# Kernel optimization log

Measured on AMD Instinct MI355X. Metric: run time of the kernel, lower is better.

## Reference

```python
import jax, jax.numpy as jnp
import numpy as np

N, L, D, H = 2, 2048, 1024, 16
Dh = D // H          # 64
HIST = 2048          # history_len
SCALE = D ** 0.5     # note: module scales by sqrt(model_dim), not sqrt(head_dim)


def setup_inputs() -> dict:
    key = jax.random.key(0)
    ks = jax.random.split(key, 10)
    f = lambda k, s, sc=1.0: jax.random.normal(k, s, dtype=jnp.float32) * sc
    i = jnp.arange(L)
    causal = i[None, :] > i[:, None]            # mask future
    old = i[None, :] <= i[:, None] - HIST       # mask beyond history window
    mask = causal | old                          # True = masked, (L, L)
    return {
        "values": f(ks[0], (N, L, D)),
        "keys": f(ks[1], (N, L, D)),
        "query": f(ks[2], (N, L, D)),
        "origin_values": f(ks[3], (N, L, D)),
        "origin_keys": f(ks[4], (N, L, D)),
        "Wv": f(ks[5], (Dh, Dh), 0.1),
        "Wk": f(ks[6], (Dh, Dh), 0.1),
        "Wq": f(ks[7], (Dh, Dh), 0.1),
        "fc_w": f(ks[8], (D, D), 0.03),
        "fc_b": jnp.zeros((D,), dtype=jnp.float32),
        "mask": mask,
    }


def reference(values, keys, query, origin_values, origin_keys, Wv, Wk, Wq, fc_w, fc_b, mask):
    # forward(..., ref_sample=True): mfpca_attention path.
    # origin_keys/values are projected exactly as the prior ref_sample=False call stored them.
    split = lambda x: x.reshape(N, L, H, Dh)
    v = split(values) @ Wv.T        # (N, L, H, Dh)  torch Linear: x @ W^T, no bias
    k = split(keys) @ Wk.T
    q = split(query) @ Wq.T
    ov = split(origin_values) @ Wv.T
    ok = split(origin_keys) @ Wk.T

    energy = jnp.einsum('nqhd,nkhd->nhqk', q, ok)       # (N, H, L, L)
    samp_energy = jnp.einsum('nlhd,nlhd->nhl', q, k)    # (N, H, L)
    eye = jnp.eye(L, dtype=bool)
    # energy.diagonal().copy_(samp_energy)
    energy = jnp.where(eye, samp_energy[:, :, None, :], energy)
    energy = jnp.where(mask, jnp.float32(-1e20), energy)
    scores = jax.nn.softmax(energy / SCALE, axis=-1)
    diag_scores = jnp.diagonal(scores, axis1=2, axis2=3)    # (N, H, L)
    scores_nodiag = jnp.where(eye, 0.0, scores)
    # NOTE: original einsum output is indexed by l (not q) -- reproduced faithfully.
    origin_attention = jnp.einsum('nhql,nlhd->nlhd', scores_nodiag, ov)
    samp_attention = jnp.einsum('nhl,nlhd->nlhd', diag_scores, v)
    attention = (samp_attention + origin_attention).reshape(N, L, D)
    return attention @ fc_w.T + fc_b
```

## Files before the change

kernel.cpp:

```cpp
#include <hip/hip_runtime.h>

#define NB 2
#define LL 2048
#define DD 1024
#define HH 16
#define NHH (NB*HH)
#define LT (LL/64)
#define KT16 (LL/16)
#define CEXP 0.0450842200277801f

typedef __bf16 bf16x8 __attribute__((ext_vector_type(8)));
typedef unsigned short u16x8 __attribute__((ext_vector_type(8)));
typedef float f32x4 __attribute__((ext_vector_type(4)));

#define MFMA16 __builtin_amdgcn_mfma_f32_16x16x32_bf16
#define EXP2 __builtin_amdgcn_exp2f

__device__ __forceinline__ unsigned short f2bf(float f) {
    unsigned u = __float_as_uint(f);
    return (unsigned short)((u + 0x7fffu + ((u >> 16) & 1u)) >> 16);
}
__device__ __forceinline__ float bf2f(unsigned short u) {
    return __uint_as_float(((unsigned)u) << 16);
}
__device__ __forceinline__ bf16x8 ldfrag(const unsigned short* p) {
    return *reinterpret_cast<const bf16x8*>(p);
}
__device__ __forceinline__ bf16x8 cvt8v(float4 a, float4 b) {
    u16x8 u;
    u[0]=f2bf(a.x); u[1]=f2bf(a.y); u[2]=f2bf(a.z); u[3]=f2bf(a.w);
    u[4]=f2bf(b.x); u[5]=f2bf(b.y); u[6]=f2bf(b.z); u[7]=f2bf(b.w);
    return __builtin_bit_cast(bf16x8, u);
}
__device__ __forceinline__ ushort4 pack4(f32x4 d, float sc) {
    ushort4 o;
    o.x = f2bf(d[0]*sc); o.y = f2bf(d[1]*sc); o.z = f2bf(d[2]*sc); o.w = f2bf(d[3]*sc);
    return o;
}
__device__ __forceinline__ void gload16(const unsigned short* g, unsigned short* l) {
    __builtin_amdgcn_global_load_lds(
        (const __attribute__((address_space(1))) unsigned int*)g,
        (__attribute__((address_space(3))) unsigned int*)l, 16, 0, 0);
}

__global__ __launch_bounds__(256) void wcvt_kernel(
    const float* __restrict__ Wk, const float* __restrict__ Wq,
    const float* __restrict__ Wv, unsigned short* __restrict__ wfrag)
{
    const int s = blockIdx.x * 256 + threadIdx.x;
    const int m = s >> 9;
    const int rem = s & 511;
    const int f = rem >> 6;
    const int lane = rem & 63;
    const int n16 = lane & 15, quad = lane >> 4;
    const int mt = f >> 1, half = f & 1;
    const float* W = (m == 0) ? Wk : (m == 1) ? Wq : Wv;
    const float* p = W + (mt*16 + n16)*64 + quad*8 + half*32;
    float4 a = *reinterpret_cast<const float4*>(p);
    float4 b = *reinterpret_cast<const float4*>(p + 4);
    *reinterpret_cast<bf16x8*>(wfrag + (size_t)s * 8) = cvt8v(a, b);
}

__global__ __launch_bounds__(256) void proj_kernel(
    const float* __restrict__ values, const float* __restrict__ keys,
    const float* __restrict__ query,  const float* __restrict__ ovals,
    const float* __restrict__ okeys,  const unsigned short* __restrict__ wfrag,
    unsigned short* __restrict__ qb, unsigned short* __restrict__ okb,
    unsigned short* __restrict__ vb, unsigned short* __restrict__ ovb,
    float* __restrict__ ediag)
{
    const int t = threadIdx.x;
    const int w = t >> 6;
    const int lane = t & 63;
    const int n16 = lane & 15;
    const int quad = lane >> 4;
    const int h = blockIdx.y;
    const int row = blockIdx.x * 64 + w * 16 + n16;
    const int nn = row >> 11;
    const int ll = row & 2047;
    const size_t xoff  = (size_t)row * DD + h * 64 + quad * 8;
    const size_t qbase = (((size_t)(nn * HH + h)) * LL + ll) * 64;
    const size_t vbase = (size_t)row * DD + h * 64;

    if (blockIdx.z == 0) {
        const float4* kp = reinterpret_cast<const float4*>(keys  + xoff);
        const float4* qp = reinterpret_cast<const float4*>(query + xoff);
        const float4* op = reinterpret_cast<const float4*>(okeys + xoff);
        float4 k0 = kp[0], k1 = kp[1], k2 = kp[8], k3 = kp[9];
        float4 q0 = qp[0], q1 = qp[1], q2 = qp[8], q3 = qp[9];
        float4 o0 = op[0], o1 = op[1], o2 = op[8], o3 = op[9];
        bf16x8 wk[8], wq[8];
#pragma unroll
        for (int f = 0; f < 8; ++f) {
            wk[f] = ldfrag(wfrag + (size_t)(f * 64 + lane) * 8);
            wq[f] = ldfrag(wfrag + (size_t)((8 + f) * 64 + lane) * 8);
        }
        bf16x8 xk0 = cvt8v(k0, k1), xk1 = cvt8v(k2, k3);
        bf16x8 xq0 = cvt8v(q0, q1), xq1 = cvt8v(q2, q3);
        bf16x8 xo0 = cvt8v(o0, o1), xo1 = cvt8v(o2, o3);
        f32x4 ka[4], qa[4];
#pragma unroll
        for (int mt = 0; mt < 4; ++mt) {
            f32x4 d = {0.f,0.f,0.f,0.f};
            d = MFMA16(wk[mt*2], xk0, d, 0,0,0);
            ka[mt] = MFMA16(wk[mt*2+1], xk1, d, 0,0,0);
        }
#pragma unroll
        for (int mt = 0; mt < 4; ++mt) {
            f32x4 d = {0.f,0.f,0.f,0.f};
            d = MFMA16(wq[mt*2], xq0, d, 0,0,0);
            qa[mt] = MFMA16(wq[mt*2+1], xq1, d, 0,0,0);
            *reinterpret_cast<ushort4*>(qb + qbase + mt*16 + quad*4) = pack4(qa[mt], CEXP);
        }
#pragma unroll
        for (int mt = 0; mt < 4; ++mt) {
            f32x4 d = {0.f,0.f,0.f,0.f};
            d = MFMA16(wk[mt*2], xo0, d, 0,0,0);
            d = MFMA16(wk[mt*2+1], xo1, d, 0,0,0);
            *reinterpret_cast<ushort4*>(okb + qbase + mt*16 + quad*4) = pack4(d, 1.0f);
        }
        float p = 0.f;
#pragma unroll
        for (int mt = 0; mt < 4; ++mt)
            p += qa[mt][0]*ka[mt][0] + qa[mt][1]*ka[mt][1]
               + qa[mt][2]*ka[mt][2] + qa[mt][3]*ka[mt][3];
        p += __shfl_xor(p, 16);
        p += __shfl_xor(p, 32);
        if (lane < 16)
            ediag[((size_t)(nn * HH + h)) * LL + ll] = p;
    } else {
        const float4* vp = reinterpret_cast<const float4*>(values + xoff);
        const float4* op = reinterpret_cast<const float4*>(ovals  + xoff);
        float4 v0 = vp[0], v1 = vp[1], v2 = vp[8], v3 = vp[9];
        float4 o0 = op[0], o1 = op[1], o2 = op[8], o3 = op[9];
        bf16x8 wv[8];
#pragma unroll
        for (int f = 0; f < 8; ++f)
            wv[f] = ldfrag(wfrag + (size_t)((16 + f) * 64 + lane) * 8);
        bf16x8 xv0 = cvt8v(v0, v1), xv1 = cvt8v(v2, v3);
        bf16x8 xo0 = cvt8v(o0, o1), xo1 = cvt8v(o2, o3);
#pragma unroll
        for (int mt = 0; mt < 4; ++mt) {
            f32x4 d = {0.f,0.f,0.f,0.f};
            d = MFMA16(wv[mt*2], xv0, d, 0,0,0);
            d = MFMA16(wv[mt*2+1], xv1, d, 0,0,0);
            *reinterpret_cast<ushort4*>(vb + vbase + mt*16 + quad*4) = pack4(d, 1.0f);
        }
#pragma unroll
        for (int mt = 0; mt < 4; ++mt) {
            f32x4 d = {0.f,0.f,0.f,0.f};
            d = MFMA16(wv[mt*2], xo0, d, 0,0,0);
            d = MFMA16(wv[mt*2+1], xo1, d, 0,0,0);
            *reinterpret_cast<ushort4*>(ovb + vbase + mt*16 + quad*4) = pack4(d, 1.0f);
        }
    }
}

__global__ __launch_bounds__(256) void zrow_part(
    const unsigned short* __restrict__ qb, const unsigned short* __restrict__ okb,
    float* __restrict__ Zbuf)
{
    const int px = blockIdx.x;
    const int pair = px >> 2;
    const int s = px & 3;
    const int nh = blockIdx.y;
    const int t = threadIdx.x;
    const int w = t >> 6;
    const int lane = t & 63;
    const int n = lane & 15;
    const int quad = lane >> 4;
    const size_t base = (size_t)nh * (LL * 64);
    const size_t nhL = (size_t)nh * LL;
    const int r0 = 4 * s + w;

#pragma unroll
    for (int half = 0; half < 2; ++half) {
        const int qt = half ? (31 - pair) : pair;
        const int kend = 4 * qt + 4;

        bf16x8 aq[4][2];
#pragma unroll
        for (int rt = 0; rt < 4; ++rt) {
            const unsigned short* p = qb + base + (size_t)(qt*64 + rt*16 + n) * 64 + quad * 8;
            aq[rt][0] = ldfrag(p); aq[rt][1] = ldfrag(p + 32);
        }

        float zacc[4][4];
#pragma unroll
        for (int rt = 0; rt < 4; ++rt)
#pragma unroll
            for (int r = 0; r < 4; ++r) zacc[rt][r] = 0.f;

        bf16x8 b0c, b1c;
        if (r0 < kend) {
            const unsigned short* kp = okb + base + (size_t)(r0*16 + n) * 64 + quad * 8;
            b0c = ldfrag(kp); b1c = ldfrag(kp + 32);
        }
        for (int kt = r0; kt < kend; kt += 16) {
            bf16x8 b0 = b0c, b1 = b1c;
            if (kt + 16 < kend) {
                const unsigned short* kp = okb + base + (size_t)((kt+16)*16 + n) * 64 + quad * 8;
                b0c = ldfrag(kp); b1c = ldfrag(kp + 32);
            }
            const int dk = kt - 4*qt;
#pragma unroll
            for (int rt = 0; rt < 4; ++rt) {
                if (rt < dk) continue;
                f32x4 d = {0.f,0.f,0.f,0.f};
                d = MFMA16(aq[rt][0], b0, d, 0,0,0);
                d = MFMA16(aq[rt][1], b1, d, 0,0,0);
                if (rt == dk) {
#pragma unroll
                    for (int r = 0; r < 4; ++r)
                        if (n < quad*4 + r) zacc[rt][r] += EXP2(d[r]);
                } else {
#pragma unroll
                    for (int r = 0; r < 4; ++r) zacc[rt][r] += EXP2(d[r]);
                }
            }
        }

#pragma unroll
        for (int rt = 0; rt < 4; ++rt)
#pragma unroll
            for (int r = 0; r < 4; ++r) {
                float z = zacc[rt][r];
                z += __shfl_xor(z, 1); z += __shfl_xor(z, 2);
                z += __shfl_xor(z, 4); z += __shfl_xor(z, 8);
                if (n == 0)
                    atomicAdd(&Zbuf[nhL + qt*64 + rt*16 + quad*4 + r], z);
            }
    }
}

__global__ __launch_bounds__(256) void zfin_kernel(
    const float* __restrict__ Zbuf, const float* __restrict__ ediag,
    float* __restrict__ invZ, float* __restrict__ diag_s)
{
    const int i = blockIdx.x * 256 + threadIdx.x;
    const float de = EXP2(ediag[i] * CEXP);
    const float iz = 1.f / (Zbuf[i] + de);
    invZ[i]   = iz;
    diag_s[i] = de * iz;
}

__global__ __launch_bounds__(256) void colsum_part(
    const unsigned short* __restrict__ qb, const unsigned short* __restrict__ okb,
    const float* __restrict__ invZ, float* __restrict__ colsum)
{
    const int px = blockIdx.x;
    const int pair = px >> 2;
    const int s = px & 3;
    const int nh = blockIdx.y;
    const int t = threadIdx.x;
    const int w = t >> 6;
    const int lane = t & 63;
    const int n = lane & 15;
    const int quad = lane >> 4;
    const size_t base = (size_t)nh * (LL * 64);
    const size_t nhL = (size_t)nh * LL;
    const int r0 = 4 * s + w;

#pragma unroll
    for (int half = 0; half < 2; ++half) {
        const int lt = half ? (31 - pair) : pair;

        bf16x8 bl[4][2];
#pragma unroll
        for (int ct = 0; ct < 4; ++ct) {
            const unsigned short* p = okb + base + (size_t)(lt*64 + ct*16 + n) * 64 + quad * 8;
            bl[ct][0] = ldfrag(p); bl[ct][1] = ldfrag(p + 32);
        }

        float cacc[4] = {0.f, 0.f, 0.f, 0.f};

        const int kstart = 4*lt + r0;
        bf16x8 a0c, a1c; float izc = 0.f;
        if (kstart < KT16) {
            const unsigned short* qp = qb + base + (size_t)(kstart*16 + n) * 64 + quad * 8;
            a0c = ldfrag(qp); a1c = ldfrag(qp + 32);
            izc = invZ[nhL + kstart*16 + n];
        }
        for (int kt = kstart; kt < KT16; kt += 16) {
            bf16x8 a0 = a0c, a1 = a1c; const float izq = izc;
            if (kt + 16 < KT16) {
                const unsigned short* qp = qb + base + (size_t)((kt+16)*16 + n) * 64 + quad * 8;
                a0c = ldfrag(qp); a1c = ldfrag(qp + 32);
                izc = invZ[nhL + (kt+16)*16 + n];
            }
            float izr[4];
#pragma unroll
            for (int r = 0; r < 4; ++r) izr[r] = __shfl(izq, quad*4 + r);
            const int dk = kt - 4*lt;
#pragma unroll
            for (int ct = 0; ct < 4; ++ct) {
                if (ct > dk) continue;
                f32x4 d = {0.f,0.f,0.f,0.f};
                d = MFMA16(a0, bl[ct][0], d, 0,0,0);
                d = MFMA16(a1, bl[ct][1], d, 0,0,0);
                if (ct == dk) {
#pragma unroll
                    for (int r = 0; r < 4; ++r)
                        if (quad*4 + r > n) cacc[ct] += EXP2(d[r]) * izr[r];
                } else {
#pragma unroll
                    for (int r = 0; r < 4; ++r) cacc[ct] += EXP2(d[r]) * izr[r];
                }
            }
        }

#pragma unroll
        for (int ct = 0; ct < 4; ++ct) {
            float c = cacc[ct];
            c += __shfl_down(c, 32);
            c += __shfl_down(c, 16);
            if (lane < 16)
                atomicAdd(&colsum[nhL + lt*64 + ct*16 + lane], c);
        }
    }
}

__global__ __launch_bounds__(256) void fcw_kernel(
    const float* __restrict__ fc_w, unsigned short* __restrict__ fcwb)
{
    const int idx = blockIdx.x * 1024 + threadIdx.x * 4;
    float4 wv = *reinterpret_cast<const float4*>(fc_w + idx);
    ushort4 o;
    o.x = f2bf(wv.x); o.y = f2bf(wv.y); o.z = f2bf(wv.z); o.w = f2bf(wv.w);
    *reinterpret_cast<ushort4*>(fcwb + idx) = o;
}

__global__ __launch_bounds__(256) void att_kernel(
    const unsigned short* __restrict__ vb, const unsigned short* __restrict__ ovb,
    const float* __restrict__ diag_s, const float* __restrict__ colsum,
    unsigned short* __restrict__ attb)
{
    const int row = blockIdx.x;
    const int nn = row >> 11, l = row & 2047;
    const int t = threadIdx.x;
    const int d0 = t * 4;
    const int h = t >> 4;
    const size_t nhl = ((size_t)(nn * HH + h)) * LL + l;
    const float ds = diag_s[nhl];
    const float cs = colsum[nhl];
    const ushort4 v  = *reinterpret_cast<const ushort4*>(vb  + (size_t)row * DD + d0);
    const ushort4 ov = *reinterpret_cast<const ushort4*>(ovb + (size_t)row * DD + d0);
    ushort4 o;
    o.x = f2bf(ds * bf2f(v.x) + cs * bf2f(ov.x));
    o.y = f2bf(ds * bf2f(v.y) + cs * bf2f(ov.y));
    o.z = f2bf(ds * bf2f(v.z) + cs * bf2f(ov.z));
    o.w = f2bf(ds * bf2f(v.w) + cs * bf2f(ov.w));
    *reinterpret_cast<ushort4*>(attb + (size_t)row * DD + d0) = o;
}

__global__ __launch_bounds__(512) void out_kernel(
    const unsigned short* __restrict__ attb, const unsigned short* __restrict__ fcwb,
    const float* __restrict__ fc_b, float* __restrict__ out)
{
    __shared__ unsigned short lds[2][2][128 * 32];

    const int bid = blockIdx.x;
    const int swz = (bid & 7) * 32 + (bid >> 3);
    const int ct = swz & 7;
    const int rt = swz >> 3;
    const int row0 = rt * 128, col0 = ct * 128;

    const int t = threadIdx.x;
    const int w = t >> 6, lane = t & 63;
    const int n = lane & 15, quad = lane >> 4;
    const int wr = w >> 2, wc = w & 3;

    const unsigned short* ga = attb + (size_t)(row0 + (t >> 2)) * DD + (t & 3) * 8;
    const unsigned short* gb = fcwb + (size_t)(col0 + (t >> 2)) * DD + (t & 3) * 8;
    unsigned short* la0 = &lds[0][0][t * 8];
    unsigned short* lb0 = &lds[0][1][t * 8];
    unsigned short* la1 = &lds[1][0][t * 8];
    unsigned short* lb1 = &lds[1][1][t * 8];

    f32x4 acc[4][2];
#pragma unroll
    for (int mt = 0; mt < 4; ++mt)
#pragma unroll
        for (int nt = 0; nt < 2; ++nt) acc[mt][nt] = (f32x4){0.f, 0.f, 0.f, 0.f};

    gload16(ga, la0);
    gload16(gb, lb0);
    __syncthreads();

    int cur = 0;
    for (int kt = 0; kt < DD / 32; ++kt) {
        if (kt + 1 < DD / 32) {
            const int kc = (kt + 1) * 32;
            gload16(ga + kc, cur ? la0 : la1);
            gload16(gb + kc, cur ? lb0 : lb1);
        }
        const unsigned short* A = &lds[cur][0][0];
        const unsigned short* B = &lds[cur][1][0];
        bf16x8 af[4], bf_[2];
#pragma unroll
        for (int mt = 0; mt < 4; ++mt)
            af[mt] = ldfrag(A + (wr * 64 + mt * 16 + n) * 32 + quad * 8);
#pragma unroll
        for (int nt = 0; nt < 2; ++nt)
            bf_[nt] = ldfrag(B + (wc * 32 + nt * 16 + n) * 32 + quad * 8);
#pragma unroll
        for (int mt = 0; mt < 4; ++mt)
#pragma unroll
            for (int nt = 0; nt < 2; ++nt)
                acc[mt][nt] = MFMA16(af[mt], bf_[nt], acc[mt][nt], 0, 0, 0);
        __syncthreads();
        cur ^= 1;
    }

#pragma unroll
    for (int nt = 0; nt < 2; ++nt) {
        const int col = col0 + wc * 32 + nt * 16 + n;
        const float bias = fc_b[col];
#pragma unroll
        for (int mt = 0; mt < 4; ++mt)
#pragma unroll
            for (int r = 0; r < 4; ++r)
                out[(size_t)(row0 + wr * 64 + mt * 16 + quad * 4 + r) * DD + col]
                    = acc[mt][nt][r] + bias;
    }
}

extern "C" void kernel_launch(void* const* d_in, const int* in_sizes, int n_in,
                              void* d_out, int out_size, void* d_ws, size_t ws_size,
                              hipStream_t stream) {
    const float* values = (const float*)d_in[0];
    const float* keys   = (const float*)d_in[1];
    const float* query  = (const float*)d_in[2];
    const float* ovals  = (const float*)d_in[3];
    const float* okeys  = (const float*)d_in[4];
    const float* Wv     = (const float*)d_in[5];
    const float* Wk     = (const float*)d_in[6];
    const float* Wq     = (const float*)d_in[7];
    const float* fc_w   = (const float*)d_in[8];
    const float* fc_b   = (const float*)d_in[9];
    float* out = (float*)d_out;

    float* ws      = (float*)d_ws;
    float* ediag   = ws;
    float* Zbuf    = ediag + 65536;
    float* colsum  = Zbuf + 65536;
    float* invZ    = colsum + 65536;
    float* diag_s  = invZ + 65536;
    unsigned short* qb   = (unsigned short*)(diag_s + 65536);
    unsigned short* okb  = qb   + 4194304;
    unsigned short* vb   = okb  + 4194304;
    unsigned short* ovb  = vb   + 4194304;
    unsigned short* attb = ovb  + 4194304;
    unsigned short* fcwb = attb + 4194304;
    unsigned short* wfrag = fcwb + 1048576;

    hipMemsetAsync(Zbuf, 0, 2 * 65536 * sizeof(float), stream);

    wcvt_kernel<<<dim3(6), 256, 0, stream>>>(Wk, Wq, Wv, wfrag);
    fcw_kernel<<<dim3(1024), 256, 0, stream>>>(fc_w, fcwb);
    proj_kernel<<<dim3(64, 16, 2), 256, 0, stream>>>(
        values, keys, query, ovals, okeys, wfrag, qb, okb, vb, ovb, ediag);
    zrow_part<<<dim3(64, NHH), 256, 0, stream>>>(qb, okb, Zbuf);
    zfin_kernel<<<dim3(256), 256, 0, stream>>>(Zbuf, ediag, invZ, diag_s);
    colsum_part<<<dim3(64, NHH), 256, 0, stream>>>(qb, okb, invZ, colsum);
    att_kernel<<<dim3(NB * LL), 256, 0, stream>>>(vb, ovb, diag_s, colsum, attb);
    out_kernel<<<dim3(256), 512, 0, stream>>>(attb, fcwb, fc_b, out);
}
```

Baseline: 266.2 us.

## Halve split factor and transpose zrow MFMA layout to cut shuffle reductions

Both the row-sum and column-sum kernels now split the key range across 2 blocks instead of 4, so each wave walks every 8th tile with double-buffered prefetch, and the grids shrink to 32 blocks per head. In zrow_part the MFMA operands are swapped so origin keys are the A operand and queries are B. Row sums then accumulate per lane and reduce with two shuffles instead of four xor-shuffles per element. colsum_part loads invZ as a float4 per quad instead of broadcasting it with shuffles. The trade-off is fewer blocks in flight (lower parallelism and fewer atomics) against more serial work per wave.

Result: faster. 239.1 us (-10.2%).

```diff
diff --git a/kernel.cpp b/kernel.cpp
--- a/kernel.cpp
+++ b/kernel.cpp
@@ -161,8 +161,8 @@
     float* __restrict__ Zbuf)
 {
     const int px = blockIdx.x;
-    const int pair = px >> 2;
-    const int s = px & 3;
+    const int pair = px >> 1;
+    const int s = px & 1;
     const int nh = blockIdx.y;
     const int t = threadIdx.x;
     const int w = t >> 6;
@@ -178,58 +178,57 @@
         const int qt = half ? (31 - pair) : pair;
         const int kend = 4 * qt + 4;
 
-        bf16x8 aq[4][2];
-#pragma unroll
-        for (int rt = 0; rt < 4; ++rt) {
-            const unsigned short* p = qb + base + (size_t)(qt*64 + rt*16 + n) * 64 + quad * 8;
-            aq[rt][0] = ldfrag(p); aq[rt][1] = ldfrag(p + 32);
-        }
-
-        float zacc[4][4];
-#pragma unroll
-        for (int rt = 0; rt < 4; ++rt)
-#pragma unroll
-            for (int r = 0; r < 4; ++r) zacc[rt][r] = 0.f;
-
-        bf16x8 b0c, b1c;
+        bf16x8 bq[4][2];
+#pragma unroll
+        for (int ct = 0; ct < 4; ++ct) {
+            const unsigned short* p = qb + base + (size_t)(qt*64 + ct*16 + n) * 64 + quad * 8;
+            bq[ct][0] = ldfrag(p); bq[ct][1] = ldfrag(p + 32);
+        }
+
+        float zacc[4] = {0.f, 0.f, 0.f, 0.f};
+
+        bf16x8 a0A = {}, a1A = {}, a0B = {}, a1B = {};
         if (r0 < kend) {
-            const unsigned short* kp = okb + base + (size_t)(r0*16 + n) * 64 + quad * 8;
-            b0c = ldfrag(kp); b1c = ldfrag(kp + 32);
-        }
-        for (int kt = r0; kt < kend; kt += 16) {
-            bf16x8 b0 = b0c, b1 = b1c;
+            const unsigned short* p = okb + base + (size_t)(r0*16 + n) * 64 + quad * 8;
+            a0A = ldfrag(p); a1A = ldfrag(p + 32);
+        }
+        if (r0 + 8 < kend) {
+            const unsigned short* p = okb + base + (size_t)((r0+8)*16 + n) * 64 + quad * 8;
+            a0B = ldfrag(p); a1B = ldfrag(p + 32);
+        }
+        for (int kt = r0; kt < kend; kt += 8) {
+            bf16x8 a0 = a0A, a1 = a1A;
+            a0A = a0B; a1A = a1B;
             if (kt + 16 < kend) {
-                const unsigned short* kp = okb + base + (size_t)((kt+16)*16 + n) * 64 + quad * 8;
-                b0c = ldfrag(kp); b1c = ldfrag(kp + 32);
+                const unsigned short* p = okb + base + (size_t)((kt+16)*16 + n) * 64 + quad * 8;
+                a0B = ldfrag(p); a1B = ldfrag(p + 32);
             }
             const int dk = kt - 4*qt;
 #pragma unroll
-            for (int rt = 0; rt < 4; ++rt) {
-                if (rt < dk) continue;
+            for (int ct = 0; ct < 4; ++ct) {
+                if (ct < dk) continue;
                 f32x4 d = {0.f,0.f,0.f,0.f};
-                d = MFMA16(aq[rt][0], b0, d, 0,0,0);
-                d = MFMA16(aq[rt][1], b1, d, 0,0,0);
-                if (rt == dk) {
+                d = MFMA16(a0, bq[ct][0], d, 0,0,0);
+                d = MFMA16(a1, bq[ct][1], d, 0,0,0);
+                if (ct == dk) {
 #pragma unroll
                     for (int r = 0; r < 4; ++r)
-                        if (n < quad*4 + r) zacc[rt][r] += EXP2(d[r]);
+                        if (quad*4 + r < n) zacc[ct] += EXP2(d[r]);
                 } else {
 #pragma unroll
-                    for (int r = 0; r < 4; ++r) zacc[rt][r] += EXP2(d[r]);
+                    for (int r = 0; r < 4; ++r) zacc[ct] += EXP2(d[r]);
                 }
             }
         }
 
 #pragma unroll
-        for (int rt = 0; rt < 4; ++rt)
-#pragma unroll
-            for (int r = 0; r < 4; ++r) {
-                float z = zacc[rt][r];
-                z += __shfl_xor(z, 1); z += __shfl_xor(z, 2);
-                z += __shfl_xor(z, 4); z += __shfl_xor(z, 8);
-                if (n == 0)
-                    atomicAdd(&Zbuf[nhL + qt*64 + rt*16 + quad*4 + r], z);
-            }
+        for (int ct = 0; ct < 4; ++ct) {
+            float z = zacc[ct];
+            z += __shfl_down(z, 32);
+            z += __shfl_down(z, 16);
+            if (lane < 16)
+                atomicAdd(&Zbuf[nhL + qt*64 + ct*16 + lane], z);
+        }
     }
 }
 
@@ -249,8 +248,8 @@
     const float* __restrict__ invZ, float* __restrict__ colsum)
 {
     const int px = blockIdx.x;
-    const int pair = px >> 2;
-    const int s = px & 3;
+    const int pair = px >> 1;
+    const int s = px & 1;
     const int nh = blockIdx.y;
     const int t = threadIdx.x;
     const int w = t >> 6;
@@ -275,22 +274,26 @@
         float cacc[4] = {0.f, 0.f, 0.f, 0.f};
 
         const int kstart = 4*lt + r0;
-        bf16x8 a0c, a1c; float izc = 0.f;
+        bf16x8 a0A = {}, a1A = {}, a0B = {}, a1B = {};
+        float4 izA = {0.f,0.f,0.f,0.f}, izB = {0.f,0.f,0.f,0.f};
         if (kstart < KT16) {
-            const unsigned short* qp = qb + base + (size_t)(kstart*16 + n) * 64 + quad * 8;
-            a0c = ldfrag(qp); a1c = ldfrag(qp + 32);
-            izc = invZ[nhL + kstart*16 + n];
-        }
-        for (int kt = kstart; kt < KT16; kt += 16) {
-            bf16x8 a0 = a0c, a1 = a1c; const float izq = izc;
+            const unsigned short* p = qb + base + (size_t)(kstart*16 + n) * 64 + quad * 8;
+            a0A = ldfrag(p); a1A = ldfrag(p + 32);
+            izA = *reinterpret_cast<const float4*>(invZ + nhL + kstart*16 + quad*4);
+        }
+        if (kstart + 8 < KT16) {
+            const unsigned short* p = qb + base + (size_t)((kstart+8)*16 + n) * 64 + quad * 8;
+            a0B = ldfrag(p); a1B = ldfrag(p + 32);
+            izB = *reinterpret_cast<const float4*>(invZ + nhL + (kstart+8)*16 + quad*4);
+        }
+        for (int kt = kstart; kt < KT16; kt += 8) {
+            bf16x8 a0 = a0A, a1 = a1A; const float4 izv = izA;
+            a0A = a0B; a1A = a1B; izA = izB;
             if (kt + 16 < KT16) {
-                const unsigned short* qp = qb + base + (size_t)((kt+16)*16 + n) * 64 + quad * 8;
-                a0c = ldfrag(qp); a1c = ldfrag(qp + 32);
-                izc = invZ[nhL + (kt+16)*16 + n];
+                const unsigned short* p = qb + base + (size_t)((kt+16)*16 + n) * 64 + quad * 8;
+                a0B = ldfrag(p); a1B = ldfrag(p + 32);
+                izB = *reinterpret_cast<const float4*>(invZ + nhL + (kt+16)*16 + quad*4);
             }
-            float izr[4];
-#pragma unroll
-            for (int r = 0; r < 4; ++r) izr[r] = __shfl(izq, quad*4 + r);
             const int dk = kt - 4*lt;
 #pragma unroll
             for (int ct = 0; ct < 4; ++ct) {
@@ -299,12 +302,15 @@
                 d = MFMA16(a0, bl[ct][0], d, 0,0,0);
                 d = MFMA16(a1, bl[ct][1], d, 0,0,0);
                 if (ct == dk) {
-#pragma unroll
-                    for (int r = 0; r < 4; ++r)
-                        if (quad*4 + r > n) cacc[ct] += EXP2(d[r]) * izr[r];
+                    if (quad*4 + 0 > n) cacc[ct] += EXP2(d[0]) * izv.x;
+                    if (quad*4 + 1 > n) cacc[ct] += EXP2(d[1]) * izv.y;
+                    if (quad*4 + 2 > n) cacc[ct] += EXP2(d[2]) * izv.z;
+                    if (quad*4 + 3 > n) cacc[ct] += EXP2(d[3]) * izv.w;
                 } else {
-#pragma unroll
-                    for (int r = 0; r < 4; ++r) cacc[ct] += EXP2(d[r]) * izr[r];
+                    cacc[ct] += EXP2(d[0]) * izv.x;
+                    cacc[ct] += EXP2(d[1]) * izv.y;
+                    cacc[ct] += EXP2(d[2]) * izv.z;
+                    cacc[ct] += EXP2(d[3]) * izv.w;
                 }
             }
         }
@@ -460,9 +466,9 @@
     fcw_kernel<<<dim3(1024), 256, 0, stream>>>(fc_w, fcwb);
     proj_kernel<<<dim3(64, 16, 2), 256, 0, stream>>>(
         values, keys, query, ovals, okeys, wfrag, qb, okb, vb, ovb, ediag);
-    zrow_part<<<dim3(64, NHH), 256, 0, stream>>>(qb, okb, Zbuf);
+    zrow_part<<<dim3(32, NHH), 256, 0, stream>>>(qb, okb, Zbuf);
     zfin_kernel<<<dim3(256), 256, 0, stream>>>(Zbuf, ediag, invZ, diag_s);
-    colsum_part<<<dim3(64, NHH), 256, 0, stream>>>(qb, okb, invZ, colsum);
+    colsum_part<<<dim3(32, NHH), 256, 0, stream>>>(qb, okb, invZ, colsum);
     att_kernel<<<dim3(NB * LL), 256, 0, stream>>>(vb, ovb, diag_s, colsum, attb);
     out_kernel<<<dim3(256), 512, 0, stream>>>(attb, fcwb, fc_b, out);
 }
```
